# Performance work log

Hardware: AMD Instinct MI355X
Metric: run time of the kernel (lower is better)

Reference implementation:

```python
import jax, jax.numpy as jnp
import numpy as np

# Concrete MACE layer instantiation: hidden irreps = F x (0e + 1o)
N, E, F, R, S, H = 20000, 320000, 64, 8, 10, 64
P = 5                      # CG tensor-product paths for (0e+1o) x (0e+1o)
AVG_NEIGH = 16.0
INV_SQRT3 = 1.0 / np.sqrt(3.0).astype(np.float32)
INV_SQRT2 = 1.0 / np.sqrt(2.0).astype(np.float32)


def setup_inputs() -> dict:
    key = jax.random.key(0)
    ks = jax.random.split(key, 24)
    rn = lambda k, shp, sc=1.0: jax.random.normal(k, shp, dtype=jnp.float32) * sc
    y = jax.random.normal(ks[2], (E, 3), dtype=jnp.float32)
    Y1 = y / jnp.linalg.norm(y, axis=-1, keepdims=True)  # unit spherical harmonics l=1
    return dict(
        s=rn(ks[0], (N, F)),                 # scalar node feats (0e)
        v=rn(ks[1], (N, F, 3)),              # vector node feats (1o)
        Y1=Y1,
        edge_feats=rn(ks[3], (E, R)),        # radial basis
        node_specie=jax.random.randint(ks[4], (N,), 0, S),
        senders=jax.random.randint(ks[5], (E,), 0, N),
        receivers=jax.random.randint(ks[6], (E,), 0, N),
        W_lin_s=rn(ks[7], (F, F), F ** -0.5),
        W_lin_v=rn(ks[8], (F, F), F ** -0.5),
        W_sc_s=rn(ks[9], (S, F, F), F ** -0.5),   # species-dependent skip
        W_sc_v=rn(ks[10], (S, F, F), F ** -0.5),
        W_rad1=rn(ks[11], (R, H), R ** -0.5),     # radial MLP
        W_rad2=rn(ks[12], (H, P * F), H ** -0.5),
        W_int_s=rn(ks[13], (F, F), F ** -0.5),    # post-aggregation linear
        W_int_v=rn(ks[14], (F, F), F ** -0.5),
        w_prod_s=rn(ks[15], (S, 5, F)),           # product-basis species weights (0e out)
        w_prod_v=rn(ks[16], (S, 4, F)),           # product-basis species weights (1o out)
        W_prod_s=rn(ks[17], (F, F), F ** -0.5),
        W_prod_v=rn(ks[18], (F, F), F ** -0.5),
        W_read=rn(ks[19], (F, 1), F ** -0.5),     # linear readout to 0e
    )


def reference(s, v, Y1, edge_feats, node_specie, senders, receivers,
              W_lin_s, W_lin_v, W_sc_s, W_sc_v, W_rad1, W_rad2,
              W_int_s, W_int_v, w_prod_s, w_prod_v, W_prod_s, W_prod_v, W_read):
    n = s.shape[0]
    # --- interaction block: linear up ---
    s1 = s @ W_lin_s                              # [N,F]
    v1 = jnp.einsum('nfc,fg->ngc', v, W_lin_v)    # [N,F,3]
    # species-dependent residual skip connection
    sc_s = jnp.einsum('nf,nfg->ng', s, W_sc_s[node_specie])
    sc_v = jnp.einsum('nfc,nfg->ngc', v, W_sc_v[node_specie])
    # radial MLP -> per-edge, per-path, per-channel tensor-product weights
    h = jax.nn.silu(edge_feats @ W_rad1)
    tw = (h @ W_rad2).reshape(-1, P, F)           # [E,P,F]
    # gather sender features onto edges
    ss = s1[senders]                              # [E,F]
    vs = v1[senders]                              # [E,F,3]
    # CG tensor product with edge spherical harmonics (Y0 == const)
    dot = jnp.einsum('efc,ec->ef', vs, Y1)        # 1o x 1o -> 0e
    crs = jnp.cross(vs, Y1[:, None, :])           # 1o x 1o -> 1o
    m_s = tw[:, 0] * ss + tw[:, 1] * dot * INV_SQRT3                     # [E,F]
    m_v = (tw[:, 2, :, None] * ss[..., None] * Y1[:, None, :]            # 0e x 1o -> 1o
           + tw[:, 3, :, None] * vs                                      # 1o x 0e -> 1o
           + tw[:, 4, :, None] * crs * INV_SQRT2)                        # [E,F,3]
    # scatter-sum over edges to receiver nodes
    A_s = jax.ops.segment_sum(m_s, receivers, num_segments=n)
    A_v = jax.ops.segment_sum(m_v, receivers, num_segments=n)
    # linear to interaction irreps + neighbor normalization (epsilon is None)
    inv = 1.0 / jnp.sqrt(jnp.asarray(AVG_NEIGH, s.dtype))
    A_s = (A_s @ W_int_s) * inv
    A_v = jnp.einsum('nfc,fg->ngc', A_v, W_int_v) * inv
    # --- equivariant product basis (symmetric contraction, correlation=3) ---
    ws = w_prod_s[node_specie]                    # [N,5,F]
    wv = w_prod_v[node_specie]                    # [N,4,F]
    d = jnp.sum(A_v * A_v, axis=-1)               # v.v invariant [N,F]
    B_s = (ws[:, 0] * A_s + ws[:, 1] * A_s * A_s + ws[:, 2] * d
           + ws[:, 3] * A_s ** 3 + ws[:, 4] * A_s * d)
    B_v = (wv[:, 0] + wv[:, 1] * A_s + wv[:, 2] * A_s * A_s + wv[:, 3] * d)[..., None] * A_v
    s_out = B_s @ W_prod_s + sc_s
    v_out = jnp.einsum('nfc,fg->ngc', B_v, W_prod_v) + sc_v
    # --- linear readout (not last layer): invariant per-node output ---
    node_outputs = s_out @ W_read                 # [N,1]
    return node_outputs, s_out, v_out
```

## Files before the change

kernel.cpp:

```cpp
#include <hip/hip_runtime.h>

#define NNODES 20000
#define NEDGES 320000
#define NTILES 1260

typedef __attribute__((ext_vector_type(8))) short short8;
typedef __attribute__((ext_vector_type(4))) float float4v;
typedef __attribute__((ext_vector_type(4))) unsigned short ushort4v;
typedef __attribute__((ext_vector_type(4))) int int4v;

#define CW2   0
#define CWls  2560
#define CWlv  3072
#define CWis  3584
#define CWiv  4096
#define CWps  4608
#define CWpv  5120
#define CWss  5632
#define CWsv  10752
#define NCHUNK_TOT 15872

__device__ __forceinline__ float bitsf(unsigned u){ union{unsigned u; float f;} x; x.u=u; return x.f; }
__device__ __forceinline__ float b2f(unsigned short u){ return bitsf(((unsigned)u)<<16); }
__device__ __forceinline__ unsigned short f2b(float f){
    union{float f; unsigned u;} x; x.f=f;
    unsigned r = x.u + 0x7fffu + ((x.u>>16)&1u);
    return (unsigned short)(r>>16);
}
__device__ __forceinline__ short8 pack8(const float* f){
    short8 r;
    #pragma unroll
    for (int j=0;j<8;++j) r[j] = (short)f2b(f[j]);
    return r;
}
__device__ __forceinline__ void atomAddF32(float* p, float v){
    asm volatile("global_atomic_add_f32 %0, %1, off" :: "v"(p), "v"(v) : "memory");
}

__constant__ float kINV_SQRT3 = 0.5773502691896258f;
__constant__ float kINV_SQRT2 = 0.7071067811865476f;
__constant__ float kINV_AVG   = 0.25f;

__global__ __launch_bounds__(256) void kprep(
    const int* __restrict__ specie,
    const float* __restrict__ Wr2,
    const float* __restrict__ Wls, const float* __restrict__ Wlv,
    const float* __restrict__ Wis, const float* __restrict__ Wiv,
    const float* __restrict__ Wps, const float* __restrict__ Wpv,
    const float* __restrict__ Wss, const float* __restrict__ Wsv,
    unsigned short* __restrict__ P,
    int* __restrict__ perm, int* __restrict__ tspec,
    int* __restrict__ ecnt)
{
    const int tid = threadIdx.x;
    for (int i = blockIdx.x*256 + tid; i < NNODES; i += 63*256) ecnt[i] = 0;

    if (blockIdx.x == 0){
        __shared__ int cnt[10], base[10], ntl[10], cur[10];
        if (tid < 10) cnt[tid] = 0;
        __syncthreads();
        for (int n = tid; n < NNODES; n += 256) atomicAdd(&cnt[specie[n]], 1);
        __syncthreads();
        if (tid == 0){
            int b = 0;
            for (int sp = 0; sp < 10; ++sp){
                base[sp] = b; cur[sp] = b;
                ntl[sp] = (cnt[sp] + 15) >> 4;
                b += ntl[sp] << 4;
            }
        }
        __syncthreads();
        for (int i = tid; i < NTILES*16; i += 256) perm[i] = -1;
        for (int t = tid; t < NTILES; t += 256){
            int sp = 0;
            #pragma unroll
            for (int k = 0; k < 10; ++k)
                if (t >= (base[k] >> 4) && t < (base[k] >> 4) + ntl[k]) sp = k;
            tspec[t] = sp;
        }
        __syncthreads();
        for (int n = tid; n < NNODES; n += 256){
            int slot = atomicAdd(&cur[specie[n]], 1);
            perm[slot] = n;
        }
        return;
    }
    const int c = (blockIdx.x - 1)*256 + tid;
    if (c >= NCHUNK_TOT) return;
    unsigned short t[8];
    if (c < 2560){
        const int nt = c >> 7, ks = (c >> 6) & 1, ln = c & 63;
        const int col = nt*16 + (ln & 15);
        const int jb  = ks*32 + ((ln >> 4) & 3)*8;
        #pragma unroll
        for (int jj = 0; jj < 8; ++jj) t[jj] = f2b(Wr2[(jb+jj)*320 + col]);
    } else {
        int c2 = c - 2560;
        const float* src;
        if      (c2 <  512){ src = Wls; }
        else if (c2 < 1024){ src = Wlv; c2 -= 512; }
        else if (c2 < 1536){ src = Wis; c2 -= 1024; }
        else if (c2 < 2048){ src = Wiv; c2 -= 1536; }
        else if (c2 < 2560){ src = Wps; c2 -= 2048; }
        else if (c2 < 3072){ src = Wpv; c2 -= 2560; }
        else if (c2 < 8192){ src = Wss; c2 -= 3072; }
        else               { src = Wsv; c2 -= 8192; }
        const int grp = c2 >> 9, loc = c2 & 511;
        const int nt = loc >> 7, ks = (loc >> 6) & 1, ln = loc & 63;
        const int col  = nt*16 + (ln & 15);
        const int row0 = grp*64 + ks*32 + ((ln>>4)&3)*8;
        #pragma unroll
        for (int jj = 0; jj < 8; ++jj) t[jj] = f2b(src[(row0+jj)*64 + col]);
    }
    unsigned* d = (unsigned*)(P + (size_t)c*8);
    d[0] = (unsigned)t[0] | ((unsigned)t[1]<<16);
    d[1] = (unsigned)t[2] | ((unsigned)t[3]<<16);
    d[2] = (unsigned)t[4] | ((unsigned)t[5]<<16);
    d[3] = (unsigned)t[6] | ((unsigned)t[7]<<16);
}

__global__ __launch_bounds__(256) void knodeA2(
    const float* __restrict__ s, const float* __restrict__ v,
    const unsigned short* __restrict__ P,
    const int* __restrict__ receivers, int* __restrict__ ecnt,
    unsigned short* __restrict__ sv1,
    unsigned short* __restrict__ s_bf, unsigned short* __restrict__ v_bf,
    float4v* __restrict__ AhZ)
{
    float4v zz = {0.f,0.f,0.f,0.f};
    for (int i = blockIdx.x*256 + threadIdx.x; i < NNODES*64; i += 313*256) AhZ[i] = zz;
    for (int e = blockIdx.x*256 + threadIdx.x; e < NEDGES; e += 313*256)
        atomicAdd(&ecnt[receivers[e]], 1);

    const int w = threadIdx.x >> 6, lane = threadIdx.x & 63;
    const int t = blockIdx.x*4 + w;
    if (t >= 1250) return;
    const int mcol = lane & 15, quad = lane >> 4;
    const int node = t*16 + mcol;
    const short8* PB = (const short8*)P;

    short8 fS[2], fV[3][2];
    #pragma unroll
    for (int ks = 0; ks < 2; ++ks){
        const int k0 = ks*32 + quad*8;
        float ts[8];
        { float4v a = *(const float4v*)&s[node*64 + k0];
          float4v b = *(const float4v*)&s[node*64 + k0 + 4];
          #pragma unroll
          for (int j = 0; j < 4; ++j){ ts[j] = a[j]; ts[4+j] = b[j]; } }
        fS[ks] = pack8(ts);
        float tv[24];
        #pragma unroll
        for (int q = 0; q < 6; ++q){
            float4v x = *(const float4v*)&v[(node*64 + k0)*3 + q*4];
            #pragma unroll
            for (int j = 0; j < 4; ++j) tv[q*4+j] = x[j];
        }
        #pragma unroll
        for (int c = 0; c < 3; ++c){
            float tc[8];
            #pragma unroll
            for (int j = 0; j < 8; ++j) tc[j] = tv[j*3 + c];
            fV[c][ks] = pack8(tc);
        }
        *(short8*)&s_bf[(size_t)node*64 + k0] = fS[ks];
        #pragma unroll
        for (int c = 0; c < 3; ++c)
            *(short8*)&v_bf[((size_t)node*3 + c)*64 + k0] = fV[c][ks];
    }
    float4v z = {0.f,0.f,0.f,0.f};
    #pragma unroll
    for (int nt = 0; nt < 4; ++nt){
        float4v aS = __builtin_amdgcn_mfma_f32_16x16x32_bf16(fS[0], PB[CWls+(nt*2+0)*64+lane], z, 0,0,0);
        aS = __builtin_amdgcn_mfma_f32_16x16x32_bf16(fS[1], PB[CWls+(nt*2+1)*64+lane], aS, 0,0,0);
        float4v aV[3];
        #pragma unroll
        for (int c = 0; c < 3; ++c){
            aV[c] = __builtin_amdgcn_mfma_f32_16x16x32_bf16(fV[c][0], PB[CWlv+(nt*2+0)*64+lane], z, 0,0,0);
            aV[c] = __builtin_amdgcn_mfma_f32_16x16x32_bf16(fV[c][1], PB[CWlv+(nt*2+1)*64+lane], aV[c], 0,0,0);
        }
        const int g = nt*16 + mcol;
        #pragma unroll
        for (int r = 0; r < 4; ++r){
            const int nr = t*16 + quad*4 + r;
            ushort4v pk = { f2b(aS[r]), f2b(aV[0][r]), f2b(aV[1][r]), f2b(aV[2][r]) };
            *(ushort4v*)&sv1[(size_t)(nr*64 + g)*4] = pk;
        }
    }
}

__global__ __launch_bounds__(256) void kscan(int* __restrict__ ecnt)
{
    __shared__ int part[256];
    const int tid = threadIdx.x;
    int4v* e4 = (int4v*)ecnt;
    const int b4 = tid*20;
    int4v c[20];
    #pragma unroll
    for (int i = 0; i < 20; ++i){
        int4v zi = {0,0,0,0};
        c[i] = (b4 + i < 5000) ? e4[b4 + i] : zi;
    }
    int sum = 0;
    #pragma unroll
    for (int i = 0; i < 20; ++i) sum += c[i][0] + c[i][1] + c[i][2] + c[i][3];
    part[tid] = sum;
    __syncthreads();
    if (tid == 0){
        int acc = 0;
        #pragma unroll 1
        for (int i = 0; i < 256; ++i){ int t = part[i]; part[i] = acc; acc += t; }
    }
    __syncthreads();
    int run = part[tid];
    #pragma unroll
    for (int i = 0; i < 20; ++i){
        int4v o;
        o[0] = run; run += c[i][0];
        o[1] = run; run += c[i][1];
        o[2] = run; run += c[i][2];
        o[3] = run; run += c[i][3];
        if (b4 + i < 5000) e4[b4 + i] = o;
    }
}

__global__ __launch_bounds__(256) void kscat(
    const int* __restrict__ receivers, int* __restrict__ ecur, int* __restrict__ eperm)
{
    const int e = blockIdx.x*256 + threadIdx.x;
    if (e >= NEDGES) return;
    const int pos = atomicAdd(&ecur[receivers[e]], 1);
    eperm[pos] = e;
}

__global__ __launch_bounds__(256, 3) void kedge2(
    const float* __restrict__ Y1, const float* __restrict__ ef,
    const int* __restrict__ senders, const int* __restrict__ receivers,
    const float* __restrict__ Wr1, const unsigned short* __restrict__ W2s,
    const unsigned short* __restrict__ sv1,
    const int* __restrict__ eperm,
    float* __restrict__ Ahf)
{
    __shared__ unsigned short hlds[64*72];
    __shared__ unsigned short twlds[64*330];
    const int lane = threadIdx.x & 63;
    const int w    = threadIdx.x >> 6;
    const int ew   = blockIdx.x*64 + w*16;

    int epreg = 0;
    if (lane < 16) epreg = eperm[ew + lane];
    const int  eme = __shfl(epreg, lane >> 2);
    const float efa = ef[eme*8 + (lane&3)*2];
    const float efb = ef[eme*8 + (lane&3)*2 + 1];

    float y0r = 0.f, y1r = 0.f, y2r = 0.f;
    int   sndreg = 0, rcvreg = 0;
    if (lane < 16){
        y0r = Y1[epreg*3 + 0];
        y1r = Y1[epreg*3 + 1];
        y2r = Y1[epreg*3 + 2];
        sndreg = senders[epreg];
        rcvreg = receivers[epreg];
    }

    ushort4v svp[16];
    #pragma unroll
    for (int e16 = 0; e16 < 16; ++e16){
        const int snd = __shfl(sndreg, e16);
        svp[e16] = *(const ushort4v*)&sv1[(size_t)(snd*64 + lane)*4];
    }

    float w1r[8];
    #pragma unroll
    for (int r = 0; r < 8; ++r) w1r[r] = Wr1[r*64 + lane];

    #pragma unroll
    for (int e16 = 0; e16 < 16; ++e16){
        float hj = 0.f;
        #pragma unroll
        for (int r = 0; r < 8; ++r)
            hj += __shfl((r&1) ? efb : efa, e16*4 + (r>>1)) * w1r[r];
        hj = hj / (1.f + __expf(-hj));
        hlds[(w*16 + e16)*72 + lane] = f2b(hj);
    }
    __syncthreads();

    short8 a0 = *(const short8*)&hlds[(w*16 + (lane&15))*72 +      (lane>>4)*8];
    short8 a1 = *(const short8*)&hlds[(w*16 + (lane&15))*72 + 32 + (lane>>4)*8];
    float4v acc[20];
    #pragma unroll
    for (int nt = 0; nt < 20; ++nt){
        short8 b0 = *(const short8*)&W2s[((nt*2+0)*64 + lane)*8];
        short8 b1 = *(const short8*)&W2s[((nt*2+1)*64 + lane)*8];
        float4v z = {0.f, 0.f, 0.f, 0.f};
        acc[nt] = __builtin_amdgcn_mfma_f32_16x16x32_bf16(a0, b0, z, 0, 0, 0);
        acc[nt] = __builtin_amdgcn_mfma_f32_16x16x32_bf16(a1, b1, acc[nt], 0, 0, 0);
    }
    #pragma unroll
    for (int nt = 0; nt < 20; ++nt){
        const int col = nt*16 + (lane & 15);
        #pragma unroll
        for (int r = 0; r < 4; ++r){
            const int erow = w*16 + (lane>>4)*4 + r;
            twlds[erow*330 + col] = f2b(acc[nt][r]);
        }
    }

    int   cur = -1;
    float aS = 0.f, aV0 = 0.f, aV1 = 0.f, aV2 = 0.f;
    #pragma unroll
    for (int e16 = 0; e16 < 16; ++e16){
        const int erow = w*16 + e16;
        float tw0 = b2f(twlds[erow*330 +   0 + lane]);
        float tw1 = b2f(twlds[erow*330 +  64 + lane]);
        float tw2 = b2f(twlds[erow*330 + 128 + lane]);
        float tw3 = b2f(twlds[erow*330 + 192 + lane]);
        float tw4 = b2f(twlds[erow*330 + 256 + lane]);
        const int rcv = __shfl(rcvreg, e16);
        float y0 = __shfl(y0r, e16);
        float y1 = __shfl(y1r, e16);
        float y2 = __shfl(y2r, e16);
        const ushort4v q = svp[e16];
        float ss  = b2f(q[0]);
        float vs0 = b2f(q[1]);
        float vs1 = b2f(q[2]);
        float vs2 = b2f(q[3]);
        float dot = vs0*y0 + vs1*y1 + vs2*y2;
        float c0 = vs1*y2 - vs2*y1;
        float c1 = vs2*y0 - vs0*y2;
        float c2 = vs0*y1 - vs1*y0;
        float ms  = tw0*ss + tw1*dot*kINV_SQRT3;
        float t2s = tw2*ss, t4 = tw4*kINV_SQRT2;
        float mv0 = t2s*y0 + tw3*vs0 + t4*c0;
        float mv1 = t2s*y1 + tw3*vs1 + t4*c1;
        float mv2 = t2s*y2 + tw3*vs2 + t4*c2;
        if (rcv != cur){
            if (cur >= 0){
                float* base = &Ahf[(size_t)cur*256 + lane];
                atomAddF32(base,       aS);
                atomAddF32(base + 64,  aV0);
                atomAddF32(base + 128, aV1);
                atomAddF32(base + 192, aV2);
            }
            cur = rcv;
            aS = 0.f; aV0 = 0.f; aV1 = 0.f; aV2 = 0.f;
        }
        aS += ms; aV0 += mv0; aV1 += mv1; aV2 += mv2;
    }
    if (cur >= 0){
        float* base = &Ahf[(size_t)cur*256 + lane];
        atomAddF32(base,       aS);
        atomAddF32(base + 64,  aV0);
        atomAddF32(base + 128, aV1);
        atomAddF32(base + 192, aV2);
    }
}

__global__ __launch_bounds__(256) void knodeC2(
    const unsigned short* __restrict__ s_bf, const unsigned short* __restrict__ v_bf,
    const float* __restrict__ Ahf,
    const unsigned short* __restrict__ P,
    const int* __restrict__ perm, const int* __restrict__ tspec,
    const float* __restrict__ wps, const float* __restrict__ wpv,
    const float* __restrict__ Wread,
    float* __restrict__ out)
{
    __shared__ unsigned short Bt[4][4][16*72];
    const int w = threadIdx.x >> 6, lane = threadIdx.x & 63;
    const int t = blockIdx.x*4 + w;
    if (t >= NTILES) return;
    const int mcol = lane & 15, quad = lane >> 4;
    const int spec = tspec[t];
    const int nA   = perm[t*16 + mcol];
    const short8* PB = (const short8*)P;
    const int sb = CWss + spec*512, vb = CWsv + spec*512;

    short8 fAs[2], fAv[3][2], fS[2], fV[3][2];
    if (nA >= 0){
        #pragma unroll
        for (int ks = 0; ks < 2; ++ks){
            const int k0 = ks*32 + quad*8;
            const float* ab = &Ahf[(size_t)nA*256 + k0];
            float as_[8], a0_[8], a1_[8], a2_[8];
            { float4v x0 = *(const float4v*)&ab[0];
              float4v x1 = *(const float4v*)&ab[4];
              #pragma unroll
              for (int j = 0; j < 4; ++j){ as_[j] = x0[j]; as_[4+j] = x1[j]; } }
            { float4v x0 = *(const float4v*)&ab[64];
              float4v x1 = *(const float4v*)&ab[68];
              #pragma unroll
              for (int j = 0; j < 4; ++j){ a0_[j] = x0[j]; a0_[4+j] = x1[j]; } }
            { float4v x0 = *(const float4v*)&ab[128];
              float4v x1 = *(const float4v*)&ab[132];
              #pragma unroll
              for (int j = 0; j < 4; ++j){ a1_[j] = x0[j]; a1_[4+j] = x1[j]; } }
            { float4v x0 = *(const float4v*)&ab[192];
              float4v x1 = *(const float4v*)&ab[196];
              #pragma unroll
              for (int j = 0; j < 4; ++j){ a2_[j] = x0[j]; a2_[4+j] = x1[j]; } }
            fAs[ks] = pack8(as_); fAv[0][ks] = pack8(a0_);
            fAv[1][ks] = pack8(a1_); fAv[2][ks] = pack8(a2_);
            fS[ks] = *(const short8*)&s_bf[(size_t)nA*64 + k0];
            #pragma unroll
            for (int c = 0; c < 3; ++c)
                fV[c][ks] = *(const short8*)&v_bf[((size_t)nA*3 + c)*64 + k0];
        }
    } else {
        short8 z8 = {};
        #pragma unroll
        for (int ks = 0; ks < 2; ++ks){
            fAs[ks] = z8; fS[ks] = z8;
            #pragma unroll
            for (int c = 0; c < 3; ++c){ fAv[c][ks] = z8; fV[c][ks] = z8; }
        }
    }

    float4v z = {0.f,0.f,0.f,0.f};
    float4v scS[4], scV[3][4];
    #pragma unroll
    for (int nt = 0; nt < 4; ++nt){
        float4v Ais = __builtin_amdgcn_mfma_f32_16x16x32_bf16(fAs[0], PB[CWis+(nt*2+0)*64+lane], z, 0,0,0);
        Ais = __builtin_amdgcn_mfma_f32_16x16x32_bf16(fAs[1], PB[CWis+(nt*2+1)*64+lane], Ais, 0,0,0);
        float4v Aiv[3];
        #pragma unroll
        for (int c = 0; c < 3; ++c){
            Aiv[c] = __builtin_amdgcn_mfma_f32_16x16x32_bf16(fAv[c][0], PB[CWiv+(nt*2+0)*64+lane], z, 0,0,0);
            Aiv[c] = __builtin_amdgcn_mfma_f32_16x16x32_bf16(fAv[c][1], PB[CWiv+(nt*2+1)*64+lane], Aiv[c], 0,0,0);
        }
        scS[nt] = __builtin_amdgcn_mfma_f32_16x16x32_bf16(fS[0], PB[sb+(nt*2+0)*64+lane], z, 0,0,0);
        scS[nt] = __builtin_amdgcn_mfma_f32_16x16x32_bf16(fS[1], PB[sb+(nt*2+1)*64+lane], scS[nt], 0,0,0);
        #pragma unroll
        for (int c = 0; c < 3; ++c){
            scV[c][nt] = __builtin_amdgcn_mfma_f32_16x16x32_bf16(fV[c][0], PB[vb+(nt*2+0)*64+lane], z, 0,0,0);
            scV[c][nt] = __builtin_amdgcn_mfma_f32_16x16x32_bf16(fV[c][1], PB[vb+(nt*2+1)*64+lane], scV[c][nt], 0,0,0);
        }
        const int g = nt*16 + mcol;
        float w0 = wps[spec*320 +   0 + g], w1 = wps[spec*320 +  64 + g];
        float w2 = wps[spec*320 + 128 + g], w3 = wps[spec*320 + 192 + g];
        float w4 = wps[spec*320 + 256 + g];
        float u0 = wpv[spec*256 +   0 + g], u1 = wpv[spec*256 +  64 + g];
        float u2 = wpv[spec*256 + 128 + g], u3 = wpv[spec*256 + 192 + g];
        #pragma unroll
        for (int r = 0; r < 4; ++r){
            float A  = Ais[r]    * kINV_AVG;
            float a0 = Aiv[0][r] * kINV_AVG;
            float a1 = Aiv[1][r] * kINV_AVG;
            float a2 = Aiv[2][r] * kINV_AVG;
            float d   = a0*a0 + a1*a1 + a2*a2;
            float as2 = A*A;
            float Bs  = w0*A + w1*as2 + w2*d + w3*as2*A + w4*A*d;
            float gg  = u0 + u1*A + u2*as2 + u3*d;
            const int row = quad*4 + r;
            Bt[w][0][row*72 + g] = f2b(Bs);
            Bt[w][1][row*72 + g] = f2b(gg*a0);
            Bt[w][2][row*72 + g] = f2b(gg*a1);
            Bt[w][3][row*72 + g] = f2b(gg*a2);
        }
    }

    short8 bS[2], bV[3][2];
    #pragma unroll
    for (int ks = 0; ks < 2; ++ks){
        bS[ks] = *(const short8*)&Bt[w][0][mcol*72 + ks*32 + quad*8];
        #pragma unroll
        for (int c = 0; c < 3; ++c)
            bV[c][ks] = *(const short8*)&Bt[w][1+c][mcol*72 + ks*32 + quad*8];
    }

    float* out_node = out;
    float* out_s    = out + NNODES;
    float* out_v    = out + NNODES + NNODES*64;
    int ndr[4];
    #pragma unroll
    for (int r = 0; r < 4; ++r) ndr[r] = perm[t*16 + quad*4 + r];
    float4v rd = {0.f,0.f,0.f,0.f};
    #pragma unroll
    for (int nt = 0; nt < 4; ++nt){
        float4v oS = scS[nt];
        oS = __builtin_amdgcn_mfma_f32_16x16x32_bf16(bS[0], PB[CWps+(nt*2+0)*64+lane], oS, 0,0,0);
        oS = __builtin_amdgcn_mfma_f32_16x16x32_bf16(bS[1], PB[CWps+(nt*2+1)*64+lane], oS, 0,0,0);
        float4v oV[3];
        #pragma unroll
        for (int c = 0; c < 3; ++c){
            oV[c] = scV[c][nt];
            oV[c] = __builtin_amdgcn_mfma_f32_16x16x32_bf16(bV[c][0], PB[CWpv+(nt*2+0)*64+lane], oV[c], 0,0,0);
            oV[c] = __builtin_amdgcn_mfma_f32_16x16x32_bf16(bV[c][1], PB[CWpv+(nt*2+1)*64+lane], oV[c], 0,0,0);
        }
        const int g = nt*16 + mcol;
        float wr = Wread[g];
        #pragma unroll
        for (int r = 0; r < 4; ++r){
            if (ndr[r] >= 0){
                out_s[ndr[r]*64 + g] = oS[r];
                #pragma unroll
                for (int c = 0; c < 3; ++c) out_v[(ndr[r]*64 + g)*3 + c] = oV[c][r];
            }
            rd[r] += oS[r] * wr;
        }
    }
    #pragma unroll
    for (int off = 1; off < 16; off <<= 1){
        #pragma unroll
        for (int r = 0; r < 4; ++r) rd[r] += __shfl_xor(rd[r], off);
    }
    if (mcol == 0){
        #pragma unroll
        for (int r = 0; r < 4; ++r) if (ndr[r] >= 0) out_node[ndr[r]] = rd[r];
    }
}

extern "C" void kernel_launch(void* const* d_in, const int* in_sizes, int n_in,
                              void* d_out, int out_size, void* d_ws, size_t ws_size,
                              hipStream_t stream)
{
    (void)in_sizes; (void)n_in; (void)out_size; (void)ws_size;
    const float* s    = (const float*)d_in[0];
    const float* v    = (const float*)d_in[1];
    const float* Y1   = (const float*)d_in[2];
    const float* ef   = (const float*)d_in[3];
    const int* specie = (const int*)d_in[4];
    const int* senders   = (const int*)d_in[5];
    const int* receivers = (const int*)d_in[6];
    const float* Wls  = (const float*)d_in[7];
    const float* Wlv  = (const float*)d_in[8];
    const float* Wss  = (const float*)d_in[9];
    const float* Wsv  = (const float*)d_in[10];
    const float* Wr1  = (const float*)d_in[11];
    const float* Wr2  = (const float*)d_in[12];
    const float* Wis  = (const float*)d_in[13];
    const float* Wiv  = (const float*)d_in[14];
    const float* wps  = (const float*)d_in[15];
    const float* wpv  = (const float*)d_in[16];
    const float* Wps  = (const float*)d_in[17];
    const float* Wpv  = (const float*)d_in[18];
    const float* Wrd  = (const float*)d_in[19];

    float* out = (float*)d_out;
    unsigned short* t_sv = (unsigned short*)(out + NNODES);
    int* ecnt  = (int*)(out + 2600000);
    int* eperm = (int*)(out + 2624000);

    char* ws = (char*)d_ws;
    unsigned short* P = (unsigned short*)ws;
    float* Ahf  = (float*)(ws + 262144);
    int* perm   = (int*)(ws + 20742144);
    int* tspec  = (int*)(ws + 20822784);
    unsigned short* s_bf = (unsigned short*)(ws + 20827824);
    unsigned short* v_bf = (unsigned short*)(ws + 23387824);

    kprep<<<63, 256, 0, stream>>>(specie, Wr2, Wls, Wlv, Wis, Wiv, Wps, Wpv, Wss, Wsv,
                                  P, perm, tspec, ecnt);
    knodeA2<<<313, 256, 0, stream>>>(s, v, P, receivers, ecnt, t_sv, s_bf, v_bf, (float4v*)Ahf);
    kscan<<<1, 256, 0, stream>>>(ecnt);
    kscat<<<1250, 256, 0, stream>>>(receivers, ecnt, eperm);
    kedge2<<<5000, 256, 0, stream>>>(Y1, ef, senders, receivers, Wr1, P + CW2*8, t_sv, eperm, Ahf);
    knodeC2<<<315, 256, 0, stream>>>(s_bf, v_bf, Ahf, P, perm, tspec, wps, wpv, Wrd, out);
}
```

Measured before the change: 320.9 us.

## Pre-permute edge Y1/senders/receivers in scatter pass; move zeroing to memset

During the counting-sort scatter, senders, receivers and Y1 are written out in receiver-sorted order, so the edge kernel reads them coalesced instead of gathering through eperm. Zeroing of the edge counts and the aggregation buffer moves to hipMemsetAsync, and the receiver histogram moves from the node kernel into the prep kernel. This removes scattered loads from the edge kernel at the cost of extra scattered writes in kscat and two extra memset launches.

```diff
diff --git a/kernel.cpp b/kernel.cpp
--- a/kernel.cpp
+++ b/kernel.cpp
@@ -43,6 +43,7 @@
 
 __global__ __launch_bounds__(256) void kprep(
     const int* __restrict__ specie,
+    const int* __restrict__ receivers,
     const float* __restrict__ Wr2,
     const float* __restrict__ Wls, const float* __restrict__ Wlv,
     const float* __restrict__ Wis, const float* __restrict__ Wiv,
@@ -53,8 +54,6 @@
     int* __restrict__ ecnt)
 {
     const int tid = threadIdx.x;
-    for (int i = blockIdx.x*256 + tid; i < NNODES; i += 63*256) ecnt[i] = 0;
-
     if (blockIdx.x == 0){
         __shared__ int cnt[10], base[10], ntl[10], cur[10];
         if (tid < 10) cnt[tid] = 0;
@@ -85,6 +84,9 @@
         }
         return;
     }
+    for (int e = (blockIdx.x - 1)*256 + tid; e < NEDGES; e += 62*256)
+        atomicAdd(&ecnt[receivers[e]], 1);
+
     const int c = (blockIdx.x - 1)*256 + tid;
     if (c >= NCHUNK_TOT) return;
     unsigned short t[8];
@@ -122,16 +124,9 @@
 __global__ __launch_bounds__(256) void knodeA2(
     const float* __restrict__ s, const float* __restrict__ v,
     const unsigned short* __restrict__ P,
-    const int* __restrict__ receivers, int* __restrict__ ecnt,
     unsigned short* __restrict__ sv1,
-    unsigned short* __restrict__ s_bf, unsigned short* __restrict__ v_bf,
-    float4v* __restrict__ AhZ)
-{
-    float4v zz = {0.f,0.f,0.f,0.f};
-    for (int i = blockIdx.x*256 + threadIdx.x; i < NNODES*64; i += 313*256) AhZ[i] = zz;
-    for (int e = blockIdx.x*256 + threadIdx.x; e < NEDGES; e += 313*256)
-        atomicAdd(&ecnt[receivers[e]], 1);
-
+    unsigned short* __restrict__ s_bf, unsigned short* __restrict__ v_bf)
+{
     const int w = threadIdx.x >> 6, lane = threadIdx.x & 63;
     const int t = blockIdx.x*4 + w;
     if (t >= 1250) return;
@@ -225,20 +220,30 @@
 }
 
 __global__ __launch_bounds__(256) void kscat(
-    const int* __restrict__ receivers, int* __restrict__ ecur, int* __restrict__ eperm)
+    const int* __restrict__ receivers, const int* __restrict__ senders,
+    const float* __restrict__ Y1,
+    int* __restrict__ ecur, int* __restrict__ eperm,
+    float* __restrict__ Y1s, int* __restrict__ snds, int* __restrict__ rcvs)
 {
     const int e = blockIdx.x*256 + threadIdx.x;
     if (e >= NEDGES) return;
-    const int pos = atomicAdd(&ecur[receivers[e]], 1);
+    const int r = receivers[e];
+    const int pos = atomicAdd(&ecur[r], 1);
     eperm[pos] = e;
+    snds[pos]  = senders[e];
+    rcvs[pos]  = r;
+    Y1s[pos*3 + 0] = Y1[e*3 + 0];
+    Y1s[pos*3 + 1] = Y1[e*3 + 1];
+    Y1s[pos*3 + 2] = Y1[e*3 + 2];
 }
 
 __global__ __launch_bounds__(256, 3) void kedge2(
-    const float* __restrict__ Y1, const float* __restrict__ ef,
-    const int* __restrict__ senders, const int* __restrict__ receivers,
+    const float* __restrict__ ef,
     const float* __restrict__ Wr1, const unsigned short* __restrict__ W2s,
     const unsigned short* __restrict__ sv1,
     const int* __restrict__ eperm,
+    const float* __restrict__ Y1s,
+    const int* __restrict__ snds, const int* __restrict__ rcvs,
     float* __restrict__ Ahf)
 {
     __shared__ unsigned short hlds[64*72];
@@ -253,15 +258,9 @@
     const float efa = ef[eme*8 + (lane&3)*2];
     const float efb = ef[eme*8 + (lane&3)*2 + 1];
 
-    float y0r = 0.f, y1r = 0.f, y2r = 0.f;
-    int   sndreg = 0, rcvreg = 0;
-    if (lane < 16){
-        y0r = Y1[epreg*3 + 0];
-        y1r = Y1[epreg*3 + 1];
-        y2r = Y1[epreg*3 + 2];
-        sndreg = senders[epreg];
-        rcvreg = receivers[epreg];
-    }
+    float yreg  = (lane < 48) ? Y1s[ew*3 + lane] : 0.f;
+    int sndreg  = (lane < 16) ? snds[ew + lane] : 0;
+    int rcvreg  = (lane < 16) ? rcvs[ew + lane] : 0;
 
     ushort4v svp[16];
     #pragma unroll
@@ -317,9 +316,9 @@
         float tw3 = b2f(twlds[erow*330 + 192 + lane]);
         float tw4 = b2f(twlds[erow*330 + 256 + lane]);
         const int rcv = __shfl(rcvreg, e16);
-        float y0 = __shfl(y0r, e16);
-        float y1 = __shfl(y1r, e16);
-        float y2 = __shfl(y2r, e16);
+        float y0 = __shfl(yreg, e16*3+0);
+        float y1 = __shfl(yreg, e16*3+1);
+        float y2 = __shfl(yreg, e16*3+2);
         const ushort4v q = svp[e16];
         float ss  = b2f(q[0]);
         float vs0 = b2f(q[1]);
@@ -537,8 +536,11 @@
 
     float* out = (float*)d_out;
     unsigned short* t_sv = (unsigned short*)(out + NNODES);
-    int* ecnt  = (int*)(out + 2600000);
-    int* eperm = (int*)(out + 2624000);
+    int*   ecnt  = (int*)(out + 2600000);
+    int*   eperm = (int*)(out + 2624000);
+    float* Y1s   = (float*)(out + 2944000);
+    int*   snds  = (int*)(out + 3904000);
+    int*   rcvs  = (int*)(out + 4224000);
 
     char* ws = (char*)d_ws;
     unsigned short* P = (unsigned short*)ws;
@@ -548,11 +550,13 @@
     unsigned short* s_bf = (unsigned short*)(ws + 20827824);
     unsigned short* v_bf = (unsigned short*)(ws + 23387824);
 
-    kprep<<<63, 256, 0, stream>>>(specie, Wr2, Wls, Wlv, Wis, Wiv, Wps, Wpv, Wss, Wsv,
-                                  P, perm, tspec, ecnt);
-    knodeA2<<<313, 256, 0, stream>>>(s, v, P, receivers, ecnt, t_sv, s_bf, v_bf, (float4v*)Ahf);
+    hipMemsetAsync(ecnt, 0, NNODES*sizeof(int), stream);
+    hipMemsetAsync(Ahf, 0, (size_t)NNODES*256*sizeof(float), stream);
+    kprep<<<63, 256, 0, stream>>>(specie, receivers, Wr2, Wls, Wlv, Wis, Wiv,
+                                  Wps, Wpv, Wss, Wsv, P, perm, tspec, ecnt);
+    knodeA2<<<313, 256, 0, stream>>>(s, v, P, t_sv, s_bf, v_bf);
     kscan<<<1, 256, 0, stream>>>(ecnt);
-    kscat<<<1250, 256, 0, stream>>>(receivers, ecnt, eperm);
-    kedge2<<<5000, 256, 0, stream>>>(Y1, ef, senders, receivers, Wr1, P + CW2*8, t_sv, eperm, Ahf);
+    kscat<<<1250, 256, 0, stream>>>(receivers, senders, Y1, ecnt, eperm, Y1s, snds, rcvs);
+    kedge2<<<5000, 256, 0, stream>>>(ef, Wr1, P + CW2*8, t_sv, eperm, Y1s, snds, rcvs, Ahf);
     knodeC2<<<315, 256, 0, stream>>>(s_bf, v_bf, Ahf, P, perm, tspec, wps, wpv, Wrd, out);
 }
```

After: 318.5 us. Within noise of the previous version (-0.7%).
